# Kernel tuning notes

Hardware: AMD Instinct MI355X
Metric: run time of the kernel (lower is better)

## Reference

```python
import jax, jax.numpy as jnp
import numpy as np


def setup_inputs() -> dict:
    key = jax.random.key(0)
    k1, k2, k3 = jax.random.split(key, 3)
    num_paths, horizon, d_obs = 1024, 64, 64
    d_input = int(d_obs + d_obs * (d_obs + 1) / 2 + 1)  # 2145
    observations = jax.random.normal(k1, (num_paths, horizon, d_obs), dtype=jnp.float32)
    weights = jax.random.normal(k2, (horizon, d_input), dtype=jnp.float32)
    biases = jax.random.normal(k3, (horizon,), dtype=jnp.float32)
    return {"observations": observations, "weights": weights, "biases": biases}


def reference(observations, weights, biases):
    # observations: [N, H, D]; weights: [H, D + D*(D+1)/2 + 1]; biases: [H]
    d_obs = observations.shape[-1]
    iu, ju = jnp.triu_indices(d_obs)  # upper-triangular (i <= j) pairs, matching the torch loop order
    quad = observations[..., iu] * observations[..., ju]      # [N, H, D*(D+1)/2]
    feats = jnp.concatenate([observations, quad], axis=-1)    # [N, H, d_input-1]
    # The torch code leaves the last feature column as zero, so weights[:, -1]
    # contributes nothing; slice it off instead of materializing a zero column.
    values = jnp.einsum("nhd,hd->nh", feats, weights[:, :-1]) + biases
    return values
```

## Files before the change

### kernel.cpp

```cpp
#include <hip/hip_runtime.h>


#define DOBS 64
#define NH   64
#define WROW 2145
#define NQUAD 2080
#define LSTR 72

typedef unsigned short u16;
typedef __attribute__((ext_vector_type(8))) short short8;
typedef __attribute__((ext_vector_type(4))) short short4v;
typedef __attribute__((ext_vector_type(4))) float floatx4;

__device__ __forceinline__ u16 f2bf(float f) {
    unsigned u = __float_as_uint(f);
    return (u16)((u + 0x7FFF + ((u >> 16) & 1)) >> 16);
}
__device__ __forceinline__ float bf2f(u16 b) {
    return __uint_as_float(((unsigned)b) << 16);
}
__device__ __forceinline__ int tri_start(int i) {
    return (i * (129 - i)) >> 1;
}

__global__ __launch_bounds__(256) void qvf_main(
    const float* __restrict__ obs, const float* __restrict__ weights,
    const float* __restrict__ biases, float* __restrict__ out, int N)
{
    __shared__ u16 O16[DOBS * LSTR];
    __shared__ u16 W16[DOBS * LSTR];
    __shared__ float LW[DOBS];

    const int h    = blockIdx.x & (NH - 1);
    const int tidx = blockIdx.x >> 6;
    const int lane = threadIdx.x & 63;
    const int wv   = threadIdx.x >> 6;
    const int n0   = tidx * 64;

    const float* __restrict__ wsrc = weights + h * WROW;

    float wq[8];
#pragma unroll
    for (int p = 0; p < 8; ++p)
        wq[p] = wsrc[DOBS + p * 256 + threadIdx.x];
    float wq8 = 0.f;
    if (threadIdx.x < NQUAD - 2048)
        wq8 = wsrc[DOBS + 2048 + threadIdx.x];

    if (threadIdx.x < DOBS) LW[threadIdx.x] = wsrc[threadIdx.x];

    {
        const short8 z = (short8)0;
        *(short8*)&W16[threadIdx.x * 8]         = z;
        *(short8*)&W16[(256 + threadIdx.x) * 8] = z;
        if (threadIdx.x < 64) *(short8*)&W16[(512 + threadIdx.x) * 8] = z;
    }

    {
        const float* __restrict__ src = obs + ((size_t)n0 * NH + h) * DOBS;
#pragma unroll
        for (int p = 0; p < 4; ++p) {
            const int g  = p * 256 + threadIdx.x;
            const int r  = g >> 4;
            const int c4 = g & 15;
            const floatx4 v = *(const floatx4*)(src + (size_t)r * (NH * DOBS) + c4 * 4);
            short4v sv;
            sv[0] = (short)f2bf(v.x); sv[1] = (short)f2bf(v.y);
            sv[2] = (short)f2bf(v.z); sv[3] = (short)f2bf(v.w);
            *(short4v*)&O16[r * LSTR + c4 * 4] = sv;
        }
    }
    __syncthreads();

#pragma unroll
    for (int p = 0; p < 9; ++p) {
        const int q = p * 256 + threadIdx.x;
        if (p == 8 && q >= NQUAD) break;
        const float v = (p < 8) ? wq[p] : wq8;
        const int   t = 16641 - 8 * q;
        int i = (int)((129.0f - __builtin_sqrtf((float)t)) * 0.5f);
        i = (i < 0) ? 0 : ((i > 63) ? 63 : i);
        if (q < tri_start(i)) --i;
        if (q >= tri_start(i + 1)) ++i;
        const int j = i + (q - tri_start(i));
        W16[i * LSTR + j] = f2bf(v);
    }
    __syncthreads();

    const int col = lane & 15;
    const int qq  = lane >> 4;
    floatx4 acc[4];
#pragma unroll
    for (int ct = 0; ct < 4; ++ct) {
        const float wl = LW[ct * 16 + col];
        acc[ct][0] = wl; acc[ct][1] = wl; acc[ct][2] = wl; acc[ct][3] = wl;
    }

    const int mrow = wv * 16 + col;
#pragma unroll
    for (int ks = 0; ks < 2; ++ks) {
        const short8 a = *(const short8*)&O16[mrow * LSTR + ks * 32 + qq * 8];
#pragma unroll
        for (int ct = 0; ct < 4; ++ct) {
            const int i = ct * 16 + col;
            const short8 b = *(const short8*)&W16[i * LSTR + ks * 32 + qq * 8];
            acc[ct] = __builtin_amdgcn_mfma_f32_16x16x32_bf16(a, b, acc[ct], 0, 0, 0);
        }
    }

    float P[4] = {0.f, 0.f, 0.f, 0.f};
#pragma unroll
    for (int ct = 0; ct < 4; ++ct) {
#pragma unroll
        for (int r = 0; r < 4; ++r) {
            const int row = wv * 16 + qq * 4 + r;
            const u16 ov = O16[row * LSTR + ct * 16 + col];
            P[r] = fmaf(acc[ct][r], bf2f(ov), P[r]);
        }
    }
#pragma unroll
    for (int msk = 1; msk < 16; msk <<= 1) {
#pragma unroll
        for (int r = 0; r < 4; ++r) P[r] += __shfl_xor(P[r], msk, 64);
    }
    if (col == 0) {
        const float b = biases[h];
#pragma unroll
        for (int r = 0; r < 4; ++r) {
            const int row = wv * 16 + qq * 4 + r;
            out[(size_t)(n0 + row) * NH + h] = P[r] + b;
        }
    }
}

extern "C" void kernel_launch(void* const* d_in, const int* in_sizes, int n_in,
                              void* d_out, int out_size, void* d_ws, size_t ws_size,
                              hipStream_t stream) {
    const float* obs     = (const float*)d_in[0];
    const float* weights = (const float*)d_in[1];
    const float* biases  = (const float*)d_in[2];
    float* out           = (float*)d_out;

    const int N = in_sizes[0] / (NH * DOBS);
    qvf_main<<<dim3((N / 64) * NH), dim3(256), 0, stream>>>(obs, weights, biases, out, N);
}
```

Baseline: 68.33 us.

## Process four path tiles per block to amortize weight scatter

Each block now handles 256 paths (four 64-row tiles) with 1024 threads instead of 64 paths with 256 threads. The per-horizon triangular weight matrix is loaded, converted and scattered into shared memory once and shared by all four tiles, so redundant weight loads and index math are cut by a factor of four. The grid shrinks to 256 blocks, which may leave compute units underused, and the larger blocks need more shared memory each.

```diff
diff --git a/kernel.cpp b/kernel.cpp
--- a/kernel.cpp
+++ b/kernel.cpp
@@ -1,11 +1,12 @@
 #include <hip/hip_runtime.h>
 
 
-#define DOBS 64
-#define NH   64
-#define WROW 2145
+#define DOBS  64
+#define NH    64
+#define WROW  2145
 #define NQUAD 2080
-#define LSTR 72
+#define LSTR  72
+#define TILES 4
 
 typedef unsigned short u16;
 typedef __attribute__((ext_vector_type(8))) short short8;
@@ -23,68 +24,62 @@
     return (i * (129 - i)) >> 1;
 }
 
-__global__ __launch_bounds__(256) void qvf_main(
+__device__ __forceinline__ void scatter_w(u16* W16, int q, float v) {
+    const int t = 16641 - 8 * q;
+    int i = (int)((129.0f - __builtin_sqrtf((float)t)) * 0.5f);
+    i = (i < 0) ? 0 : ((i > 63) ? 63 : i);
+    if (q < tri_start(i)) --i;
+    if (q >= tri_start(i + 1)) ++i;
+    const int j = i + (q - tri_start(i));
+    W16[i * LSTR + j] = f2bf(v);
+}
+
+__global__ __launch_bounds__(1024) void qvf_main(
     const float* __restrict__ obs, const float* __restrict__ weights,
     const float* __restrict__ biases, float* __restrict__ out, int N)
 {
-    __shared__ u16 O16[DOBS * LSTR];
+    __shared__ u16 O16[TILES][DOBS * LSTR];
     __shared__ u16 W16[DOBS * LSTR];
     __shared__ float LW[DOBS];
 
+    const int tid  = threadIdx.x;
     const int h    = blockIdx.x & (NH - 1);
-    const int tidx = blockIdx.x >> 6;
-    const int lane = threadIdx.x & 63;
-    const int wv   = threadIdx.x >> 6;
-    const int n0   = tidx * 64;
+    const int sup  = blockIdx.x >> 6;
+    const int n0   = sup * (TILES * 64);
+    const int lane = tid & 63;
+    const int wv   = tid >> 6;
+    const int tile = wv >> 2;
+    const int strip= wv & 3;
 
     const float* __restrict__ wsrc = weights + h * WROW;
 
-    float wq[8];
-#pragma unroll
-    for (int p = 0; p < 8; ++p)
-        wq[p] = wsrc[DOBS + p * 256 + threadIdx.x];
-    float wq8 = 0.f;
-    if (threadIdx.x < NQUAD - 2048)
-        wq8 = wsrc[DOBS + 2048 + threadIdx.x];
+    const float wq0 = wsrc[DOBS + tid];
+    const float wq1 = wsrc[DOBS + 1024 + tid];
+    const float wq2 = (tid < NQUAD - 2048) ? wsrc[DOBS + 2048 + tid] : 0.f;
 
-    if (threadIdx.x < DOBS) LW[threadIdx.x] = wsrc[threadIdx.x];
+    if (tid < DOBS) LW[tid] = wsrc[tid];
+
+    if (tid < 576) *(short8*)&W16[tid * 8] = (short8)0;
 
     {
-        const short8 z = (short8)0;
-        *(short8*)&W16[threadIdx.x * 8]         = z;
-        *(short8*)&W16[(256 + threadIdx.x) * 8] = z;
-        if (threadIdx.x < 64) *(short8*)&W16[(512 + threadIdx.x) * 8] = z;
-    }
-
-    {
-        const float* __restrict__ src = obs + ((size_t)n0 * NH + h) * DOBS;
+        const float* __restrict__ osrc = obs + ((size_t)n0 * NH + h) * DOBS;
 #pragma unroll
-        for (int p = 0; p < 4; ++p) {
-            const int g  = p * 256 + threadIdx.x;
-            const int r  = g >> 4;
-            const int c4 = g & 15;
-            const floatx4 v = *(const floatx4*)(src + (size_t)r * (NH * DOBS) + c4 * 4);
+        for (int p = 0; p < TILES; ++p) {
+            const int r  = (tid >> 4) & 63;
+            const int c4 = tid & 15;
+            const floatx4 v = *(const floatx4*)(
+                osrc + (size_t)(p * 64 + r) * (NH * DOBS) + c4 * 4);
             short4v sv;
             sv[0] = (short)f2bf(v.x); sv[1] = (short)f2bf(v.y);
             sv[2] = (short)f2bf(v.z); sv[3] = (short)f2bf(v.w);
-            *(short4v*)&O16[r * LSTR + c4 * 4] = sv;
+            *(short4v*)&O16[p][r * LSTR + c4 * 4] = sv;
         }
     }
     __syncthreads();
 
-#pragma unroll
-    for (int p = 0; p < 9; ++p) {
-        const int q = p * 256 + threadIdx.x;
-        if (p == 8 && q >= NQUAD) break;
-        const float v = (p < 8) ? wq[p] : wq8;
-        const int   t = 16641 - 8 * q;
-        int i = (int)((129.0f - __builtin_sqrtf((float)t)) * 0.5f);
-        i = (i < 0) ? 0 : ((i > 63) ? 63 : i);
-        if (q < tri_start(i)) --i;
-        if (q >= tri_start(i + 1)) ++i;
-        const int j = i + (q - tri_start(i));
-        W16[i * LSTR + j] = f2bf(v);
-    }
+    scatter_w(W16, tid, wq0);
+    scatter_w(W16, 1024 + tid, wq1);
+    if (tid < NQUAD - 2048) scatter_w(W16, 2048 + tid, wq2);
     __syncthreads();
 
     const int col = lane & 15;
@@ -96,10 +91,11 @@
         acc[ct][0] = wl; acc[ct][1] = wl; acc[ct][2] = wl; acc[ct][3] = wl;
     }
 
-    const int mrow = wv * 16 + col;
+    const u16* __restrict__ Ot = O16[tile];
+    const int mrow = strip * 16 + col;
 #pragma unroll
     for (int ks = 0; ks < 2; ++ks) {
-        const short8 a = *(const short8*)&O16[mrow * LSTR + ks * 32 + qq * 8];
+        const short8 a = *(const short8*)&Ot[mrow * LSTR + ks * 32 + qq * 8];
 #pragma unroll
         for (int ct = 0; ct < 4; ++ct) {
             const int i = ct * 16 + col;
@@ -113,8 +109,8 @@
     for (int ct = 0; ct < 4; ++ct) {
 #pragma unroll
         for (int r = 0; r < 4; ++r) {
-            const int row = wv * 16 + qq * 4 + r;
-            const u16 ov = O16[row * LSTR + ct * 16 + col];
+            const int row = strip * 16 + qq * 4 + r;
+            const u16 ov = Ot[row * LSTR + ct * 16 + col];
             P[r] = fmaf(acc[ct][r], bf2f(ov), P[r]);
         }
     }
@@ -127,8 +123,8 @@
         const float b = biases[h];
 #pragma unroll
         for (int r = 0; r < 4; ++r) {
-            const int row = wv * 16 + qq * 4 + r;
-            out[(size_t)(n0 + row) * NH + h] = P[r] + b;
+            const int row = strip * 16 + qq * 4 + r;
+            out[(size_t)(n0 + tile * 64 + row) * NH + h] = P[r] + b;
         }
     }
 }
@@ -142,5 +138,6 @@
     float* out           = (float*)d_out;
 
     const int N = in_sizes[0] / (NH * DOBS);
-    qvf_main<<<dim3((N / 64) * NH), dim3(256), 0, stream>>>(obs, weights, biases, out, N);
+    qvf_main<<<dim3((N / (64 * TILES)) * NH), dim3(1024), 0, stream>>>(
+        obs, weights, biases, out, N);
 }
```

Result: no change. 68.47 us (+0.2%).
